# Optimization experiments

Hardware: AMD Instinct MI355X
Metric: run time of the kernel (lower is better)

Reference implementation:

```python
import jax, jax.numpy as jnp
import numpy as np

N, K, C, OUT = 2048, 14, 512, 512
SCALE = 4.0
BN_EPS = 1e-5


def _edge_lists(k):
    # pairs i<j with i,j != k-1 and adj[i,j] > 0 (adj is fully connected ones)
    ei, ej = [], []
    for i in range(k - 1):
        for j in range(i + 1, k - 1):
            ei.append(i)
            ej.append(j)
    return np.asarray(ei, np.int32), np.asarray(ej, np.int32)


def setup_inputs() -> dict:
    key = jax.random.key(0)
    k0, k1, k2, k3 = jax.random.split(key, 4)
    ei, ej = _edge_lists(K)
    std = 0.02
    return {
        "inputs": jax.random.normal(k0, (N, K, C), dtype=jnp.float32),
        "adj": jnp.ones((K, K), dtype=jnp.float32),
        "edge_i": jnp.asarray(ei),
        "edge_j": jnp.asarray(ej),
        "gamma": jnp.ones((C,), dtype=jnp.float32),
        "beta": jnp.zeros((C,), dtype=jnp.float32),
        "w_direct": jax.random.normal(k1, (C,), dtype=jnp.float32) * std,
        "W_merged": jax.random.normal(k2, (OUT, C), dtype=jnp.float32) * std,
        "W_orig": jax.random.normal(k3, (OUT, C), dtype=jnp.float32) * std,
    }


def reference(inputs, adj, edge_i, edge_j, gamma, beta, w_direct, W_merged, W_orig):
    n, k, c = inputs.shape
    # --- learn_adj ---
    global_feat = inputs[:, k - 1 : k, :]                      # [N,1,c]
    distances = jnp.abs(inputs - global_feat)                  # [N,k,c]
    # pairwise gaps only on the static edge list (i<j, non-global, adj>0)
    gap = 15.0 * (distances[:, edge_i, :] - distances[:, edge_j, :])  # [N,E,c]
    # BatchNorm1d over channel c, batch stats over (N, E), biased variance
    mean = jnp.mean(gap, axis=(0, 1))
    var = jnp.mean(jnp.square(gap - mean), axis=(0, 1))
    bn = (gap - mean) * (gamma / jnp.sqrt(var + BN_EPS)) + beta        # [N,E,c]
    a = jax.nn.sigmoid(SCALE * jnp.einsum("nec,c->ne", bn, w_direct))  # [N,E]
    adj2 = jnp.ones((n, k, k), dtype=inputs.dtype)
    adj2 = adj2.at[:, edge_i, edge_j].set(2.0 * a)
    adj2 = adj2.at[:, edge_j, edge_i].set(2.0 * (1.0 - a))
    new_adj = adj2 * adj[None, :, :]
    norm = jnp.sum(jnp.abs(new_adj), axis=2, keepdims=True)    # L1 row norm
    new_adj = new_adj / jnp.maximum(norm, 1e-12)
    # --- graph conv ---
    agg = jnp.einsum("nij,njc->nic", new_adj, inputs)          # [N,k,c]
    merged = jax.nn.relu(jnp.einsum("nkc,oc->nko", agg, W_merged))
    original = jnp.einsum("nkc,oc->nko", inputs, W_orig)
    return merged + original
```

## Files before the change

### kernel.cpp

```cpp
#include <hip/hip_runtime.h>
#include <stdint.h>

#define K_NODES 14
#define C_DIM   512
#define OUT_DIM 512
#define N_EDGE  78

typedef float  f32x4  __attribute__((ext_vector_type(4)));
typedef __bf16 bf16x8 __attribute__((ext_vector_type(8)));

__device__ __forceinline__ unsigned short f2bf(float f) {
    unsigned int u = __builtin_bit_cast(unsigned int, f);
    unsigned int r = (u + 0x7fffu + ((u >> 16) & 1u)) >> 16;
    return (unsigned short)r;
}
__device__ __forceinline__ float bf2f(unsigned short s) {
    return __builtin_bit_cast(float, (unsigned int)s << 16);
}

__device__ __forceinline__ void async16(const void* g, void* l) {
    __builtin_amdgcn_global_load_lds(
        (const __attribute__((address_space(1))) unsigned int*)g,
        (__attribute__((address_space(3))) unsigned int*)l, 16, 0, 0);
}

__global__ __launch_bounds__(512) void stats_partial(
    const float* __restrict__ x, float* __restrict__ part,
    unsigned short* __restrict__ xbf, int n_per_block,
    const float* __restrict__ Wm, const float* __restrict__ Wo,
    unsigned short* __restrict__ wmbf, unsigned short* __restrict__ wobf)
{
    int t  = threadIdx.x;
    int q  = t & 127;
    int sn = t >> 7;
    int n0 = blockIdx.x * n_per_block;
    float as0=0.f,as1=0.f,as2=0.f,as3=0.f;
    float aq0=0.f,aq1=0.f,aq2=0.f,aq3=0.f;
    for (int nn = sn; nn < n_per_block; nn += 4) {
        size_t base = (size_t)(n0 + nn) * K_NODES * C_DIM + q * 4;
        f32x4 g = *(const f32x4*)(x + base + 13 * C_DIM);
        ushort4 gb; gb.x=f2bf(g.x); gb.y=f2bf(g.y); gb.z=f2bf(g.z); gb.w=f2bf(g.w);
        *(ushort4*)(xbf + base + 13 * C_DIM) = gb;
        float S10=0,S11=0,S12=0,S13=0, S20=0,S21=0,S22=0,S23=0, Sw0=0,Sw1=0,Sw2=0,Sw3=0;
        #pragma unroll
        for (int k = 0; k < 13; ++k) {
            f32x4 v = *(const f32x4*)(x + base + k * C_DIM);
            ushort4 vb; vb.x=f2bf(v.x); vb.y=f2bf(v.y); vb.z=f2bf(v.z); vb.w=f2bf(v.w);
            *(ushort4*)(xbf + base + k * C_DIM) = vb;
            float wk = (float)(12 - 2 * k);
            float d0=fabsf(v.x-g.x), d1=fabsf(v.y-g.y), d2=fabsf(v.z-g.z), d3=fabsf(v.w-g.w);
            S10+=d0; S11+=d1; S12+=d2; S13+=d3;
            S20+=d0*d0; S21+=d1*d1; S22+=d2*d2; S23+=d3*d3;
            Sw0+=wk*d0; Sw1+=wk*d1; Sw2+=wk*d2; Sw3+=wk*d3;
        }
        as0 += 15.f*Sw0; as1 += 15.f*Sw1; as2 += 15.f*Sw2; as3 += 15.f*Sw3;
        aq0 += 225.f*(13.f*S20 - S10*S10); aq1 += 225.f*(13.f*S21 - S11*S11);
        aq2 += 225.f*(13.f*S22 - S12*S12); aq3 += 225.f*(13.f*S23 - S13*S13);
    }
    __shared__ f32x4 redS[4][128];
    __shared__ f32x4 redQ[4][128];
    redS[sn][q] = (f32x4){as0, as1, as2, as3};
    redQ[sn][q] = (f32x4){aq0, aq1, aq2, aq3};
    __syncthreads();
    if (sn == 0) {
        f32x4 s = redS[0][q] + redS[1][q] + redS[2][q] + redS[3][q];
        f32x4 z = redQ[0][q] + redQ[1][q] + redQ[2][q] + redQ[3][q];
        *(f32x4*)(part + (size_t)blockIdx.x * 1024 + q * 4)       = s;
        *(f32x4*)(part + (size_t)blockIdx.x * 1024 + 512 + q * 4) = z;
    }
    int i0 = blockIdx.x * 1024 + t;
    wmbf[i0]       = f2bf(Wm[i0]);
    wmbf[i0 + 512] = f2bf(Wm[i0 + 512]);
    wobf[i0]       = f2bf(Wo[i0]);
    wobf[i0 + 512] = f2bf(Wo[i0 + 512]);
}

__global__ __launch_bounds__(1024) void finalize_stats(
    const float* __restrict__ part, float inv_ne,
    const float* __restrict__ gamma, const float* __restrict__ beta,
    const float* __restrict__ wdir, float* __restrict__ u, float* __restrict__ bconst)
{
    int c = threadIdx.x & 511;
    int h = threadIdx.x >> 9;
    float s = 0.f, q = 0.f;
    for (int b = h * 128; b < h * 128 + 128; b += 16) {
        #pragma unroll
        for (int t = 0; t < 16; ++t) {
            s += part[(size_t)(b + t) * 1024 + c];
            q += part[(size_t)(b + t) * 1024 + 512 + c];
        }
    }
    __shared__ float sh_s[512], sh_q[512], red[512];
    if (h == 0) { sh_s[c] = s; sh_q[c] = q; }
    __syncthreads();
    if (h == 1) { sh_s[c] += s; sh_q[c] += q; }
    __syncthreads();
    if (h == 0) {
        float mean = sh_s[c] * inv_ne;
        float var  = sh_q[c] * inv_ne - mean * mean;
        float sc   = gamma[c] / sqrtf(var + 1e-5f);
        u[c] = sc * wdir[c];
        red[c] = (beta[c] - mean * sc) * wdir[c];
    }
    __syncthreads();
    for (int st = 256; st > 0; st >>= 1) {
        if (threadIdx.x < st) red[threadIdx.x] += red[threadIdx.x + st];
        __syncthreads();
    }
    if (threadIdx.x == 0) *bconst = red[0];
}

__global__ __launch_bounds__(256) void fuse_graph(
    const unsigned short* __restrict__ xbf, const float* __restrict__ adj,
    const int* __restrict__ ei, const int* __restrict__ ej,
    const float* __restrict__ u, const float* __restrict__ bconst,
    unsigned short* __restrict__ aggbf)
{
    __shared__ float WL[4][196];
    __shared__ float DlL[4][16];
    __shared__ float invL[4][16];
    int wv = threadIdx.x >> 6, lane = threadIdx.x & 63;
    int n = blockIdx.x * 4 + wv;
    size_t base = (size_t)n * K_NODES * C_DIM + lane * 8;

    float xf[K_NODES][8];
    #pragma unroll
    for (int k = 0; k < K_NODES; ++k) {
        uint4 raw = *(const uint4*)(xbf + base + k * C_DIM);
        unsigned int w0=raw.x, w1=raw.y, w2=raw.z, w3=raw.w;
        xf[k][0]=bf2f(w0&0xffff); xf[k][1]=bf2f(w0>>16);
        xf[k][2]=bf2f(w1&0xffff); xf[k][3]=bf2f(w1>>16);
        xf[k][4]=bf2f(w2&0xffff); xf[k][5]=bf2f(w2>>16);
        xf[k][6]=bf2f(w3&0xffff); xf[k][7]=bf2f(w3>>16);
    }
    f32x4 u0 = *(const f32x4*)(u + lane * 8);
    f32x4 u1 = *(const f32x4*)(u + lane * 8 + 4);
    float uc[8] = {u0.x,u0.y,u0.z,u0.w,u1.x,u1.y,u1.z,u1.w};

    #pragma unroll
    for (int k = 0; k < 13; ++k) {
        float p = 0.f;
        #pragma unroll
        for (int j = 0; j < 8; ++j) p += fabsf(xf[k][j] - xf[13][j]) * uc[j];
        #pragma unroll
        for (int off = 1; off < 64; off <<= 1) p += __shfl_xor(p, off, 64);
        if (lane == 0) DlL[wv][k] = p;
    }
    __syncthreads();

    #pragma unroll
    for (int e = 0; e < 4; ++e) {
        int idx = e * 64 + lane;
        if (idx < 196) WL[wv][idx] = adj[idx];
    }
    __syncthreads();
    for (int e = lane; e < N_EDGE; e += 64) {
        int ii = ei[e], jj = ej[e];
        float z = 4.0f * (15.f * (DlL[wv][ii] - DlL[wv][jj]) + *bconst);
        float a = 1.f / (1.f + expf(-z));
        WL[wv][ii * K_NODES + jj] *= 2.f * a;
        WL[wv][jj * K_NODES + ii] *= 2.f * (1.f - a);
    }
    __syncthreads();
    if (lane < K_NODES) {
        float s = 0.f;
        #pragma unroll
        for (int j = 0; j < K_NODES; ++j) s += fabsf(WL[wv][lane * K_NODES + j]);
        invL[wv][lane] = 1.f / fmaxf(s, 1e-12f);
    }
    __syncthreads();

    #pragma unroll
    for (int i = 0; i < K_NODES; ++i) {
        float s[8] = {0,0,0,0,0,0,0,0};
        #pragma unroll
        for (int j = 0; j < K_NODES; ++j) {
            float w = WL[wv][i * K_NODES + j];
            #pragma unroll
            for (int c = 0; c < 8; ++c) s[c] += w * xf[j][c];
        }
        float wi = invL[wv][i];
        uint4 r;
        r.x = (unsigned int)f2bf(s[0]*wi) | ((unsigned int)f2bf(s[1]*wi) << 16);
        r.y = (unsigned int)f2bf(s[2]*wi) | ((unsigned int)f2bf(s[3]*wi) << 16);
        r.z = (unsigned int)f2bf(s[4]*wi) | ((unsigned int)f2bf(s[5]*wi) << 16);
        r.w = (unsigned int)f2bf(s[6]*wi) | ((unsigned int)f2bf(s[7]*wi) << 16);
        *(uint4*)(aggbf + base + i * C_DIM) = r;
    }
}

#define TM 128
#define TN 128
#define BK 64

__global__ __launch_bounds__(256) void gemm_fused(
    const unsigned short* __restrict__ Aagg, const unsigned short* __restrict__ Axin,
    const unsigned short* __restrict__ Bwm,  const unsigned short* __restrict__ Bwo,
    float* __restrict__ out)
{
    __shared__ unsigned short lA[TM * BK];
    __shared__ unsigned short lB[TN * BK];
    int tid  = threadIdx.x;
    int lane = tid & 63;
    int wave = tid >> 6;
    int wr = wave >> 1, wc = wave & 1;
    int bm = blockIdx.x * TM;
    int bn = blockIdx.y * TN;

    f32x4 acc[4][4];
    #pragma unroll
    for (int i = 0; i < 4; ++i)
        #pragma unroll
        for (int j = 0; j < 4; ++j) acc[i][j] = (f32x4){0.f, 0.f, 0.f, 0.f};

    int lrow = lane & 15;
    int xorv = lane & 7;
    int srow  = tid >> 3;
    int lcu   = ((tid & 7) ^ (srow & 7)) * 8;

    #pragma unroll
    for (int pass = 0; pass < 2; ++pass) {
        const unsigned short* A = pass ? Axin : Aagg;
        const unsigned short* B = pass ? Bwo  : Bwm;
        for (int kb = 0; kb < C_DIM; kb += BK) {
            __syncthreads();
            #pragma unroll
            for (int it = 0; it < 4; ++it) {
                int row = it * 32 + srow;
                async16(A + (size_t)(bm + row) * C_DIM + kb + lcu,
                        &lA[(size_t)(it * 256 + wave * 64) * 8]);
                async16(B + (size_t)(bn + row) * C_DIM + kb + lcu,
                        &lB[(size_t)(it * 256 + wave * 64) * 8]);
            }
            __syncthreads();
            #pragma unroll
            for (int ks = 0; ks < 2; ++ks) {
                int pchunk = ((ks * 4 + (lane >> 4)) ^ xorv) * 8;
                bf16x8 af[4], bfr[4];
                #pragma unroll
                for (int i = 0; i < 4; ++i)
                    af[i] = *(const bf16x8*)&lA[(wr * 64 + i * 16 + lrow) * BK + pchunk];
                #pragma unroll
                for (int j = 0; j < 4; ++j)
                    bfr[j] = *(const bf16x8*)&lB[(wc * 64 + j * 16 + lrow) * BK + pchunk];
                #pragma unroll
                for (int i = 0; i < 4; ++i)
                    #pragma unroll
                    for (int j = 0; j < 4; ++j)
                        acc[i][j] = __builtin_amdgcn_mfma_f32_16x16x32_bf16(
                            af[i], bfr[j], acc[i][j], 0, 0, 0);
            }
        }
        if (pass == 0) {
            #pragma unroll
            for (int i = 0; i < 4; ++i)
                #pragma unroll
                for (int j = 0; j < 4; ++j)
                    #pragma unroll
                    for (int r = 0; r < 4; ++r)
                        acc[i][j][r] = fmaxf(acc[i][j][r], 0.f);
        }
    }

    int orow0 = bm + wr * 64 + (lane >> 4) * 4;
    int ocol0 = bn + wc * 64 + (lane & 15);
    #pragma unroll
    for (int i = 0; i < 4; ++i)
        #pragma unroll
        for (int j = 0; j < 4; ++j)
            #pragma unroll
            for (int r = 0; r < 4; ++r)
                out[(size_t)(orow0 + i * 16 + r) * OUT_DIM + (ocol0 + j * 16)] = acc[i][j][r];
}

extern "C" void kernel_launch(void* const* d_in, const int* in_sizes, int n_in,
                              void* d_out, int out_size, void* d_ws, size_t ws_size,
                              hipStream_t stream)
{
    const float* x     = (const float*)d_in[0];
    const float* adj   = (const float*)d_in[1];
    const int*   ei    = (const int*)d_in[2];
    const int*   ej    = (const int*)d_in[3];
    const float* gamma = (const float*)d_in[4];
    const float* beta  = (const float*)d_in[5];
    const float* wdir  = (const float*)d_in[6];
    const float* Wm    = (const float*)d_in[7];
    const float* Wo    = (const float*)d_in[8];
    float* out = (float*)d_out;

    int N = in_sizes[0] / (K_NODES * C_DIM);
    int M = N * K_NODES;

    float* ws_f   = (float*)d_ws;
    float* u      = ws_f + 1024;
    float* bconst = ws_f + 1536;
    float* part   = ws_f + 2048;
    char*  wsb    = (char*)d_ws;
    size_t off    = (size_t)(2048 + 256 * 1024) * sizeof(float);
    unsigned short* wmbf  = (unsigned short*)(wsb + off);  off += (size_t)OUT_DIM * C_DIM * 2;
    unsigned short* wobf  = (unsigned short*)(wsb + off);  off += (size_t)OUT_DIM * C_DIM * 2;
    unsigned short* xbf   = (unsigned short*)(wsb + off);  off += (size_t)M * C_DIM * 2;
    unsigned short* aggbf = (unsigned short*)(wsb + off);

    const int stats_blocks = 256;
    int n_per_block = N / stats_blocks;
    float inv_ne = 1.0f / ((float)N * (float)N_EDGE);

    hipLaunchKernelGGL(stats_partial, dim3(stats_blocks), dim3(512), 0, stream,
                       x, part, xbf, n_per_block, Wm, Wo, wmbf, wobf);
    hipLaunchKernelGGL(finalize_stats, dim3(1), dim3(1024), 0, stream,
                       part, inv_ne, gamma, beta, wdir, u, bconst);
    hipLaunchKernelGGL(fuse_graph, dim3(N / 4), dim3(256), 0, stream,
                       xbf, adj, ei, ej, u, bconst, aggbf);
    hipLaunchKernelGGL(gemm_fused, dim3(M / TM, OUT_DIM / TN), dim3(256), 0, stream,
                       aggbf, xbf, wmbf, wobf, out);
}
```

Measured before the change: 193.5 us.

## Split per-sample work across more threads in stats and graph-fuse kernels

The stats kernel now uses 1024-thread blocks with one sample per 128-thread group and no per-thread loop. It relies on N/8 = 256 blocks, so the partial-sum layout stays unchanged. fuse_graph now gives each sample two waves, each covering half the channels, which halves the per-thread register array (xf 14x8 to 14x4). The two half-channel partial distances are combined in LDS, and the adjacency build is split across the two waves. The aim is more parallelism and occupancy in exchange for more blocks and somewhat more reduction work per sample.

Result: no change. 191.4 us (-1.1%).

```diff
diff --git a/kernel.cpp b/kernel.cpp
--- a/kernel.cpp
+++ b/kernel.cpp
@@ -24,55 +24,53 @@
         (__attribute__((address_space(3))) unsigned int*)l, 16, 0, 0);
 }
 
-__global__ __launch_bounds__(512) void stats_partial(
+__global__ __launch_bounds__(1024) void stats_partial(
     const float* __restrict__ x, float* __restrict__ part,
-    unsigned short* __restrict__ xbf, int n_per_block,
+    unsigned short* __restrict__ xbf,
     const float* __restrict__ Wm, const float* __restrict__ Wo,
     unsigned short* __restrict__ wmbf, unsigned short* __restrict__ wobf)
 {
     int t  = threadIdx.x;
     int q  = t & 127;
     int sn = t >> 7;
-    int n0 = blockIdx.x * n_per_block;
-    float as0=0.f,as1=0.f,as2=0.f,as3=0.f;
-    float aq0=0.f,aq1=0.f,aq2=0.f,aq3=0.f;
-    for (int nn = sn; nn < n_per_block; nn += 4) {
-        size_t base = (size_t)(n0 + nn) * K_NODES * C_DIM + q * 4;
-        f32x4 g = *(const f32x4*)(x + base + 13 * C_DIM);
-        ushort4 gb; gb.x=f2bf(g.x); gb.y=f2bf(g.y); gb.z=f2bf(g.z); gb.w=f2bf(g.w);
-        *(ushort4*)(xbf + base + 13 * C_DIM) = gb;
-        float S10=0,S11=0,S12=0,S13=0, S20=0,S21=0,S22=0,S23=0, Sw0=0,Sw1=0,Sw2=0,Sw3=0;
-        #pragma unroll
-        for (int k = 0; k < 13; ++k) {
-            f32x4 v = *(const f32x4*)(x + base + k * C_DIM);
-            ushort4 vb; vb.x=f2bf(v.x); vb.y=f2bf(v.y); vb.z=f2bf(v.z); vb.w=f2bf(v.w);
-            *(ushort4*)(xbf + base + k * C_DIM) = vb;
-            float wk = (float)(12 - 2 * k);
-            float d0=fabsf(v.x-g.x), d1=fabsf(v.y-g.y), d2=fabsf(v.z-g.z), d3=fabsf(v.w-g.w);
-            S10+=d0; S11+=d1; S12+=d2; S13+=d3;
-            S20+=d0*d0; S21+=d1*d1; S22+=d2*d2; S23+=d3*d3;
-            Sw0+=wk*d0; Sw1+=wk*d1; Sw2+=wk*d2; Sw3+=wk*d3;
-        }
-        as0 += 15.f*Sw0; as1 += 15.f*Sw1; as2 += 15.f*Sw2; as3 += 15.f*Sw3;
-        aq0 += 225.f*(13.f*S20 - S10*S10); aq1 += 225.f*(13.f*S21 - S11*S11);
-        aq2 += 225.f*(13.f*S22 - S12*S12); aq3 += 225.f*(13.f*S23 - S13*S13);
-    }
-    __shared__ f32x4 redS[4][128];
-    __shared__ f32x4 redQ[4][128];
-    redS[sn][q] = (f32x4){as0, as1, as2, as3};
-    redQ[sn][q] = (f32x4){aq0, aq1, aq2, aq3};
+    int n  = blockIdx.x * 8 + sn;
+    size_t base = (size_t)n * K_NODES * C_DIM + q * 4;
+
+    f32x4 g = *(const f32x4*)(x + base + 13 * C_DIM);
+    ushort4 gb; gb.x=f2bf(g.x); gb.y=f2bf(g.y); gb.z=f2bf(g.z); gb.w=f2bf(g.w);
+    *(ushort4*)(xbf + base + 13 * C_DIM) = gb;
+
+    float S10=0,S11=0,S12=0,S13=0, S20=0,S21=0,S22=0,S23=0, Sw0=0,Sw1=0,Sw2=0,Sw3=0;
+    #pragma unroll
+    for (int k = 0; k < 13; ++k) {
+        f32x4 v = *(const f32x4*)(x + base + k * C_DIM);
+        ushort4 vb; vb.x=f2bf(v.x); vb.y=f2bf(v.y); vb.z=f2bf(v.z); vb.w=f2bf(v.w);
+        *(ushort4*)(xbf + base + k * C_DIM) = vb;
+        float wk = (float)(12 - 2 * k);
+        float d0=fabsf(v.x-g.x), d1=fabsf(v.y-g.y), d2=fabsf(v.z-g.z), d3=fabsf(v.w-g.w);
+        S10+=d0; S11+=d1; S12+=d2; S13+=d3;
+        S20+=d0*d0; S21+=d1*d1; S22+=d2*d2; S23+=d3*d3;
+        Sw0+=wk*d0; Sw1+=wk*d1; Sw2+=wk*d2; Sw3+=wk*d3;
+    }
+    f32x4 as = (f32x4){15.f*Sw0, 15.f*Sw1, 15.f*Sw2, 15.f*Sw3};
+    f32x4 aq = (f32x4){225.f*(13.f*S20 - S10*S10), 225.f*(13.f*S21 - S11*S11),
+                       225.f*(13.f*S22 - S12*S12), 225.f*(13.f*S23 - S13*S13)};
+
+    __shared__ f32x4 redS[8][128];
+    __shared__ f32x4 redQ[8][128];
+    redS[sn][q] = as;
+    redQ[sn][q] = aq;
     __syncthreads();
     if (sn == 0) {
-        f32x4 s = redS[0][q] + redS[1][q] + redS[2][q] + redS[3][q];
-        f32x4 z = redQ[0][q] + redQ[1][q] + redQ[2][q] + redQ[3][q];
+        f32x4 s = redS[0][q], z = redQ[0][q];
+        #pragma unroll
+        for (int r = 1; r < 8; ++r) { s += redS[r][q]; z += redQ[r][q]; }
         *(f32x4*)(part + (size_t)blockIdx.x * 1024 + q * 4)       = s;
         *(f32x4*)(part + (size_t)blockIdx.x * 1024 + 512 + q * 4) = z;
     }
     int i0 = blockIdx.x * 1024 + t;
-    wmbf[i0]       = f2bf(Wm[i0]);
-    wmbf[i0 + 512] = f2bf(Wm[i0 + 512]);
-    wobf[i0]       = f2bf(Wo[i0]);
-    wobf[i0 + 512] = f2bf(Wo[i0 + 512]);
+    wmbf[i0] = f2bf(Wm[i0]);
+    wobf[i0] = f2bf(Wo[i0]);
 }
 
 __global__ __launch_bounds__(1024) void finalize_stats(
@@ -116,76 +114,72 @@
     const float* __restrict__ u, const float* __restrict__ bconst,
     unsigned short* __restrict__ aggbf)
 {
-    __shared__ float WL[4][196];
-    __shared__ float DlL[4][16];
-    __shared__ float invL[4][16];
+    __shared__ float WL[2][196];
+    __shared__ float Dp[2][2][13];
+    __shared__ float invL[2][14];
     int wv = threadIdx.x >> 6, lane = threadIdx.x & 63;
-    int n = blockIdx.x * 4 + wv;
-    size_t base = (size_t)n * K_NODES * C_DIM + lane * 8;
-
-    float xf[K_NODES][8];
+    int sp = wv >> 1;
+    int h  = wv & 1;
+    int n  = blockIdx.x * 2 + sp;
+    size_t base = (size_t)n * K_NODES * C_DIM + h * 256 + lane * 4;
+
+    float xf[K_NODES][4];
     #pragma unroll
     for (int k = 0; k < K_NODES; ++k) {
-        uint4 raw = *(const uint4*)(xbf + base + k * C_DIM);
-        unsigned int w0=raw.x, w1=raw.y, w2=raw.z, w3=raw.w;
-        xf[k][0]=bf2f(w0&0xffff); xf[k][1]=bf2f(w0>>16);
-        xf[k][2]=bf2f(w1&0xffff); xf[k][3]=bf2f(w1>>16);
-        xf[k][4]=bf2f(w2&0xffff); xf[k][5]=bf2f(w2>>16);
-        xf[k][6]=bf2f(w3&0xffff); xf[k][7]=bf2f(w3>>16);
-    }
-    f32x4 u0 = *(const f32x4*)(u + lane * 8);
-    f32x4 u1 = *(const f32x4*)(u + lane * 8 + 4);
-    float uc[8] = {u0.x,u0.y,u0.z,u0.w,u1.x,u1.y,u1.z,u1.w};
+        uint2 raw = *(const uint2*)(xbf + base + k * C_DIM);
+        xf[k][0]=bf2f(raw.x&0xffff); xf[k][1]=bf2f(raw.x>>16);
+        xf[k][2]=bf2f(raw.y&0xffff); xf[k][3]=bf2f(raw.y>>16);
+    }
+    f32x4 uv = *(const f32x4*)(u + h * 256 + lane * 4);
 
     #pragma unroll
     for (int k = 0; k < 13; ++k) {
-        float p = 0.f;
-        #pragma unroll
-        for (int j = 0; j < 8; ++j) p += fabsf(xf[k][j] - xf[13][j]) * uc[j];
+        float p = fabsf(xf[k][0]-xf[13][0])*uv.x + fabsf(xf[k][1]-xf[13][1])*uv.y
+                + fabsf(xf[k][2]-xf[13][2])*uv.z + fabsf(xf[k][3]-xf[13][3])*uv.w;
         #pragma unroll
         for (int off = 1; off < 64; off <<= 1) p += __shfl_xor(p, off, 64);
-        if (lane == 0) DlL[wv][k] = p;
-    }
-    __syncthreads();
-
-    #pragma unroll
-    for (int e = 0; e < 4; ++e) {
-        int idx = e * 64 + lane;
-        if (idx < 196) WL[wv][idx] = adj[idx];
-    }
-    __syncthreads();
-    for (int e = lane; e < N_EDGE; e += 64) {
-        int ii = ei[e], jj = ej[e];
-        float z = 4.0f * (15.f * (DlL[wv][ii] - DlL[wv][jj]) + *bconst);
-        float a = 1.f / (1.f + expf(-z));
-        WL[wv][ii * K_NODES + jj] *= 2.f * a;
-        WL[wv][jj * K_NODES + ii] *= 2.f * (1.f - a);
-    }
-    __syncthreads();
-    if (lane < K_NODES) {
+        if (lane == 0) Dp[sp][h][k] = p;
+    }
+    __syncthreads();
+
+    if (h == 0) {
+        for (int e = lane; e < N_EDGE; e += 64) {
+            int ii = ei[e], jj = ej[e];
+            float Di = Dp[sp][0][ii] + Dp[sp][1][ii];
+            float Dj = Dp[sp][0][jj] + Dp[sp][1][jj];
+            float z = 4.0f * (15.f * (Di - Dj) + *bconst);
+            float a = 1.f / (1.f + expf(-z));
+            WL[sp][ii * K_NODES + jj] = adj[ii * K_NODES + jj] * (2.f * a);
+            WL[sp][jj * K_NODES + ii] = adj[jj * K_NODES + ii] * (2.f * (1.f - a));
+        }
+    } else {
+        for (int idx = lane; idx < K_NODES * K_NODES; idx += 64) {
+            int i = idx / K_NODES, j = idx - i * K_NODES;
+            if (i == j || i == 13 || j == 13) WL[sp][idx] = adj[idx];
+        }
+    }
+    __syncthreads();
+    if (h == 0 && lane < K_NODES) {
         float s = 0.f;
         #pragma unroll
-        for (int j = 0; j < K_NODES; ++j) s += fabsf(WL[wv][lane * K_NODES + j]);
-        invL[wv][lane] = 1.f / fmaxf(s, 1e-12f);
+        for (int j = 0; j < K_NODES; ++j) s += fabsf(WL[sp][lane * K_NODES + j]);
+        invL[sp][lane] = 1.f / fmaxf(s, 1e-12f);
     }
     __syncthreads();
 
     #pragma unroll
     for (int i = 0; i < K_NODES; ++i) {
-        float s[8] = {0,0,0,0,0,0,0,0};
+        float s0=0.f,s1=0.f,s2=0.f,s3=0.f;
         #pragma unroll
         for (int j = 0; j < K_NODES; ++j) {
-            float w = WL[wv][i * K_NODES + j];
-            #pragma unroll
-            for (int c = 0; c < 8; ++c) s[c] += w * xf[j][c];
-        }
-        float wi = invL[wv][i];
-        uint4 r;
-        r.x = (unsigned int)f2bf(s[0]*wi) | ((unsigned int)f2bf(s[1]*wi) << 16);
-        r.y = (unsigned int)f2bf(s[2]*wi) | ((unsigned int)f2bf(s[3]*wi) << 16);
-        r.z = (unsigned int)f2bf(s[4]*wi) | ((unsigned int)f2bf(s[5]*wi) << 16);
-        r.w = (unsigned int)f2bf(s[6]*wi) | ((unsigned int)f2bf(s[7]*wi) << 16);
-        *(uint4*)(aggbf + base + i * C_DIM) = r;
+            float w = WL[sp][i * K_NODES + j];
+            s0 += w*xf[j][0]; s1 += w*xf[j][1]; s2 += w*xf[j][2]; s3 += w*xf[j][3];
+        }
+        float wi = invL[sp][i];
+        uint2 r;
+        r.x = (unsigned int)f2bf(s0*wi) | ((unsigned int)f2bf(s1*wi) << 16);
+        r.y = (unsigned int)f2bf(s2*wi) | ((unsigned int)f2bf(s3*wi) << 16);
+        *(uint2*)(aggbf + base + i * C_DIM) = r;
     }
 }
 
@@ -302,15 +296,13 @@
     unsigned short* xbf   = (unsigned short*)(wsb + off);  off += (size_t)M * C_DIM * 2;
     unsigned short* aggbf = (unsigned short*)(wsb + off);
 
-    const int stats_blocks = 256;
-    int n_per_block = N / stats_blocks;
     float inv_ne = 1.0f / ((float)N * (float)N_EDGE);
 
-    hipLaunchKernelGGL(stats_partial, dim3(stats_blocks), dim3(512), 0, stream,
-                       x, part, xbf, n_per_block, Wm, Wo, wmbf, wobf);
+    hipLaunchKernelGGL(stats_partial, dim3(N / 8), dim3(1024), 0, stream,
+                       x, part, xbf, Wm, Wo, wmbf, wobf);
     hipLaunchKernelGGL(finalize_stats, dim3(1), dim3(1024), 0, stream,
                        part, inv_ne, gamma, beta, wdir, u, bconst);
-    hipLaunchKernelGGL(fuse_graph, dim3(N / 4), dim3(256), 0, stream,
+    hipLaunchKernelGGL(fuse_graph, dim3(N / 2), dim3(256), 0, stream,
                        xbf, adj, ei, ej, u, bconst, aggbf);
     hipLaunchKernelGGL(gemm_fused, dim3(M / TM, OUT_DIM / TN), dim3(256), 0, stream,
                        aggbf, xbf, wmbf, wobf, out);
```
